# Optimization experiments

Measured on AMD Instinct MI355X. Metric: run time of the kernel, lower is better.

## Reference

```python
import jax, jax.numpy as jnp
import numpy as np
from jax import lax

IMG = 800.0
PRE_NMS = 2000
POST_NMS = 1000
IOU_T = 0.7
BBOX_XFORM_CLIP = float(np.log(1000.0 / 16.0))


def build_anchors():
    # torchvision FPN anchor generator: one size per level, 3 aspect ratios
    strides = [4, 8, 16, 32, 64]
    sizes = [32, 64, 128, 256, 512]
    ratios = [0.5, 1.0, 2.0]
    out = []
    for s, sz in zip(strides, sizes):
        f = int(np.ceil(800 / s))  # feature map side
        base = []
        for r in ratios:
            w = sz * np.sqrt(1.0 / r)
            h = sz * np.sqrt(r)
            base.append([-w / 2, -h / 2, w / 2, h / 2])
        base = np.asarray(base)  # [3,4]
        sx = (np.arange(f) + 0.5) * s
        sy = (np.arange(f) + 0.5) * s
        yy, xx = np.meshgrid(sy, sx, indexing='ij')
        shifts = np.stack([xx, yy, xx, yy], -1).reshape(-1, 1, 4)
        out.append((shifts + base).reshape(-1, 4))
    return np.concatenate(out, 0).astype(np.float32)  # [159882,4]


def setup_inputs() -> dict:
    key = jax.random.key(0)
    k1, k2 = jax.random.split(key)
    B = 16
    anchors = jnp.asarray(build_anchors())
    A = anchors.shape[0]
    scores = jax.random.normal(k1, (B, A), dtype=jnp.float32)
    deltas = jax.random.normal(k2, (B, A, 4), dtype=jnp.float32) * 0.1
    return {"scores": scores, "deltas": deltas, "anchors": anchors}


def decode_boxes(deltas, anchors):
    wa = anchors[:, 2] - anchors[:, 0]
    ha = anchors[:, 3] - anchors[:, 1]
    cxa = anchors[:, 0] + 0.5 * wa
    cya = anchors[:, 1] + 0.5 * ha
    dx, dy = deltas[:, 0], deltas[:, 1]
    dw = jnp.minimum(deltas[:, 2], BBOX_XFORM_CLIP)
    dh = jnp.minimum(deltas[:, 3], BBOX_XFORM_CLIP)
    cx = dx * wa + cxa
    cy = dy * ha + cya
    w = jnp.exp(dw) * wa
    h = jnp.exp(dh) * ha
    boxes = jnp.stack([cx - 0.5 * w, cy - 0.5 * h, cx + 0.5 * w, cy + 0.5 * h], -1)
    return jnp.clip(boxes, 0.0, IMG)


def box_iou(a, b):
    # a: [N,4], b: [M,4]
    area_a = (a[:, 2] - a[:, 0]) * (a[:, 3] - a[:, 1])
    area_b = (b[:, 2] - b[:, 0]) * (b[:, 3] - b[:, 1])
    lt = jnp.maximum(a[:, None, :2], b[None, :, :2])
    rb = jnp.minimum(a[:, None, 2:], b[None, :, 2:])
    wh = jnp.clip(rb - lt, 0.0)
    inter = wh[..., 0] * wh[..., 1]
    return inter / (area_a[:, None] + area_b[None, :] - inter + 1e-9)


def greedy_nms_keep(boxes, iou_t):
    # boxes are sorted by descending score
    K = boxes.shape[0]
    iou = box_iou(boxes, boxes)  # [K,K]
    idx = jnp.arange(K)

    def body(i, keep):
        sup = (iou[i] > iou_t) & keep[i] & (idx > i)
        return keep & ~sup

    return lax.fori_loop(0, K, body, jnp.ones((K,), bool))


def _process_image(scores_i, deltas_i, anchors):
    # top-k pre-NMS on objectness logits (torchvision RPN order)
    top_logits, idx = lax.top_k(scores_i, PRE_NMS)
    boxes = decode_boxes(deltas_i[idx], anchors[idx])  # [PRE,4]
    keep = greedy_nms_keep(boxes, IOU_T)
    masked = jnp.where(keep, top_logits, -jnp.inf)
    kept_logits, idx2 = lax.top_k(masked, POST_NMS)
    kept_boxes = boxes[idx2]
    valid = jnp.isfinite(kept_logits)
    probs = jax.nn.sigmoid(jnp.where(valid, kept_logits, 0.0))
    out_boxes = jnp.where(valid[:, None], kept_boxes, 0.0)
    out_scores = jnp.where(valid, probs, 0.0)
    return jnp.concatenate([out_boxes, out_scores[:, None]], -1)  # [POST,5]


def reference(scores, deltas, anchors):
    return jax.vmap(_process_image, in_axes=(0, 0, None))(scores, deltas, anchors)
```

## Files before the change

### kernel.cpp

```cpp
#include <hip/hip_runtime.h>
#include <math.h>

#define PRE_NMS 2000
#define POST_NMS 1000
#define IOU_T 0.7f
#define IMGSZ 800.0f
#define CAP 6144
#define SORTN 2048
#define NBINS 1024
#define NWORDS 32
#define NSLICE 16
#define MROWS 2048

typedef unsigned long long u64;

__device__ __forceinline__ unsigned key_of(float f) {
    unsigned u = __float_as_uint(f);
    return (u & 0x80000000u) ? ~u : (u | 0x80000000u);
}
__device__ __forceinline__ float inv_key(unsigned k) {
    unsigned u = (k & 0x80000000u) ? (k ^ 0x80000000u) : ~k;
    return __uint_as_float(u);
}

__global__ __launch_bounds__(256) void hist_kernel(
    const float* __restrict__ scores, int A, unsigned* __restrict__ ghist) {
  int b = blockIdx.x, slice = blockIdx.y;
  __shared__ unsigned h[NBINS];
  int tid = threadIdx.x;
  for (int i = tid; i < NBINS; i += 256) h[i] = 0;
  __syncthreads();
  int per = (A + NSLICE - 1) / NSLICE;
  int lo = slice * per, hi = min(lo + per, A);
  const float* sc = scores + (size_t)b * A;
  for (int i = lo + tid; i < hi; i += 256)
    atomicAdd(&h[key_of(sc[i]) >> 22], 1u);
  __syncthreads();
  for (int i = tid; i < NBINS; i += 256)
    if (h[i]) atomicAdd(&ghist[b * NBINS + i], h[i]);
}

__global__ __launch_bounds__(256) void compact_kernel(
    const float* __restrict__ scores, int A, const unsigned* __restrict__ ghist,
    u64* __restrict__ cand, int* __restrict__ cand_cnt, int* __restrict__ T1) {
  int b = blockIdx.x, slice = blockIdx.y;
  int tid = threadIdx.x;
  int lane = tid & 63, wave = tid >> 6;
  __shared__ unsigned sa[2][NBINS];
  __shared__ int sT;
  for (int i = tid; i < NBINS; i += 256) sa[0][i] = ghist[b * NBINS + i];
  __syncthreads();
  int src = 0;
  for (int d = 1; d < NBINS; d <<= 1) {
    for (int i = tid; i < NBINS; i += 256)
      sa[src ^ 1][i] = sa[src][i] + ((i + d < NBINS) ? sa[src][i + d] : 0u);
    __syncthreads();
    src ^= 1;
  }
  for (int i = tid; i < NBINS; i += 256) {
    unsigned v = sa[src][i];
    unsigned nx = (i < NBINS - 1) ? sa[src][i + 1] : 0u;
    if (v >= PRE_NMS && nx < PRE_NMS) sT = i;
  }
  __syncthreads();
  int T = sT;
  if (slice == 0 && tid == 0) T1[b] = T;
  int per = (A + NSLICE - 1) / NSLICE;
  int lo = slice * per, hi = min(lo + per, A);
  const float* sc = scores + (size_t)b * A;
  int cnt = 0;
  for (int i = lo + tid; i < hi; i += 256)
    cnt += ((int)(key_of(sc[i]) >> 22) >= T);
  int pfx = cnt;
  #pragma unroll
  for (int d = 1; d < 64; d <<= 1) {
    int t2 = __shfl_up(pfx, d, 64);
    if (lane >= d) pfx += t2;
  }
  __shared__ int s_wt[4];
  __shared__ int s_base;
  if (lane == 63) s_wt[wave] = pfx;
  __syncthreads();
  if (tid == 0) {
    int tot = s_wt[0] + s_wt[1] + s_wt[2] + s_wt[3];
    int acc = 0;
    #pragma unroll
    for (int w2 = 0; w2 < 4; ++w2) { int t3 = s_wt[w2]; s_wt[w2] = acc; acc += t3; }
    s_base = atomicAdd(&cand_cnt[b], tot);
  }
  __syncthreads();
  int my_off = s_base + s_wt[wave] + (pfx - cnt);
  u64* cb = cand + (size_t)b * CAP;
  for (int i = lo + tid; i < hi; i += 256) {
    unsigned k = key_of(sc[i]);
    if ((int)(k >> 22) >= T) {
      if (my_off < CAP) cb[my_off] = ((u64)k << 32) | (unsigned)(~i);
      my_off++;
    }
  }
}

__global__ __launch_bounds__(1024) void refine_select_kernel(
    const u64* __restrict__ cand, const int* __restrict__ cand_cnt,
    const int* __restrict__ T1,
    u64* __restrict__ gsel, int* __restrict__ sel_cnt) {
  int b = blockIdx.x, tid = threadIdx.x;
  int lane = tid & 63;
  __shared__ unsigned h2[NBINS];
  __shared__ unsigned tmp[NBINS];
  __shared__ int s_above, s_sel, s_T2;
  int n = min(cand_cnt[b], CAP);
  const u64* cb = cand + (size_t)b * CAP;
  h2[tid] = 0;
  if (tid == 0) { s_above = 0; s_sel = 0; }
  __syncthreads();
  int T1v = T1[b];
  int loc = 0;
  for (int i = tid; i < n; i += 1024) {
    unsigned k = (unsigned)(cb[i] >> 32);
    if ((int)(k >> 22) > T1v) loc++;
    else atomicAdd(&h2[(k >> 12) & 1023], 1u);
  }
  for (int d = 32; d; d >>= 1) loc += __shfl_down(loc, d, 64);
  if (lane == 0 && loc) atomicAdd(&s_above, loc);
  __syncthreads();
  unsigned v = h2[tid];
  for (int d = 1; d < NBINS; d <<= 1) {
    tmp[tid] = v;
    __syncthreads();
    if (tid + d < NBINS) v += tmp[tid + d];
    __syncthreads();
  }
  tmp[tid] = v;
  __syncthreads();
  int above = s_above;
  unsigned nextv = (tid < NBINS - 1) ? tmp[tid + 1] : 0u;
  if (above + (int)v >= PRE_NMS && above + (int)nextv < PRE_NMS) s_T2 = tid;
  __syncthreads();
  unsigned thresh20 = ((unsigned)T1v << 10) | (unsigned)s_T2;
  u64* gs = gsel + (size_t)b * SORTN;
  for (int i = tid; i < n; i += 1024) {
    u64 cv = cb[i];
    if ((unsigned)(cv >> 44) >= thresh20) {
      int pos = atomicAdd(&s_sel, 1);
      if (pos < SORTN) gs[pos] = cv;
    }
  }
  __syncthreads();
  if (tid == 0) sel_cnt[b] = min(s_sel, SORTN);
}

__global__ __launch_bounds__(256) void rank_decode_kernel(
    const u64* __restrict__ gsel, const int* __restrict__ sel_cnt,
    const float* __restrict__ deltas, const float* __restrict__ anchors, int A,
    float* __restrict__ boxes, float* __restrict__ topk_logit) {
  int b = blockIdx.x, ci = blockIdx.y;
  int tid = threadIdx.x;
  __shared__ u64 keys[SORTN];
  const u64* gs = gsel + (size_t)b * SORTN;
  int n = sel_cnt[b];
  for (int i = tid; i < SORTN; i += 256)
    keys[i] = (i < n) ? gs[i] : 0ULL;
  __syncthreads();
  int i = ci * 256 + tid;
  u64 my = keys[i];
  int rank = 0;
  const ulonglong2* k2 = (const ulonglong2*)keys;
  #pragma unroll 4
  for (int j = 0; j < SORTN / 2; ++j) {
    ulonglong2 kk = k2[j];
    rank += (kk.x > my) + (kk.y > my);
  }
  if (i < n && rank < PRE_NMS) {
    int a = (int)(~(unsigned)my);
    topk_logit[b * PRE_NMS + rank] = inv_key((unsigned)(my >> 32));
    const float CLIP = 4.135166556742356f;
    float4 dl = ((const float4*)deltas)[(size_t)b * A + a];
    float4 an = ((const float4*)anchors)[a];
    float wa = __fsub_rn(an.z, an.x);
    float ha = __fsub_rn(an.w, an.y);
    float cxa = __fadd_rn(an.x, __fmul_rn(0.5f, wa));
    float cya = __fadd_rn(an.y, __fmul_rn(0.5f, ha));
    float dw = fminf(dl.z, CLIP), dh = fminf(dl.w, CLIP);
    float cx = __fadd_rn(__fmul_rn(dl.x, wa), cxa);
    float cy = __fadd_rn(__fmul_rn(dl.y, ha), cya);
    float w2 = __fmul_rn((float)exp((double)dw), wa);
    float h2f = __fmul_rn((float)exp((double)dh), ha);
    float x1 = __fsub_rn(cx, __fmul_rn(0.5f, w2));
    float y1 = __fsub_rn(cy, __fmul_rn(0.5f, h2f));
    float x2 = __fadd_rn(cx, __fmul_rn(0.5f, w2));
    float y2 = __fadd_rn(cy, __fmul_rn(0.5f, h2f));
    x1 = fminf(fmaxf(x1, 0.f), IMGSZ);
    y1 = fminf(fmaxf(y1, 0.f), IMGSZ);
    x2 = fminf(fmaxf(x2, 0.f), IMGSZ);
    y2 = fminf(fmaxf(y2, 0.f), IMGSZ);
    ((float4*)boxes)[(size_t)b * PRE_NMS + rank] = make_float4(x1, y1, x2, y2);
  }
}

__global__ __launch_bounds__(64) void iou_tile(
    const float* __restrict__ boxes, u64* __restrict__ maskT) {
  int k = blockIdx.x;
  int b = blockIdx.y;
  int wj = (int)((sqrtf(8.0f * k + 1.0f) - 1.0f) * 0.5f);
  while ((wj + 1) * (wj + 2) / 2 <= k) ++wj;
  while (wj * (wj + 1) / 2 > k) --wj;
  int ti = k - wj * (wj + 1) / 2;
  int lane = threadIdx.x;
  int i = ti * 64 + lane;
  const float4* bb = (const float4*)boxes + (size_t)b * PRE_NMS;
  __shared__ float4 sbox[64];
  int jg = wj * 64 + lane;
  sbox[lane] = bb[min(jg, PRE_NMS - 1)];
  float4 A4 = bb[min(i, PRE_NMS - 1)];
  __syncthreads();
  float area_a = __fmul_rn(__fsub_rn(A4.z, A4.x), __fsub_rn(A4.w, A4.y));
  u64 m = 0;
  #pragma unroll 8
  for (int jj = 0; jj < 64; ++jj) {
    float4 Bb = sbox[jj];
    float area_b = __fmul_rn(__fsub_rn(Bb.z, Bb.x), __fsub_rn(Bb.w, Bb.y));
    float ltx = fmaxf(A4.x, Bb.x), lty = fmaxf(A4.y, Bb.y);
    float rbx = fminf(A4.z, Bb.z), rby = fminf(A4.w, Bb.w);
    float iw = fmaxf(__fsub_rn(rbx, ltx), 0.f);
    float ih = fmaxf(__fsub_rn(rby, lty), 0.f);
    float inter = __fmul_rn(iw, ih);
    float denom = __fadd_rn(__fsub_rn(__fadd_rn(area_a, area_b), inter), 1e-9f);
    float iou = inter / denom;
    int j = wj * 64 + jj;
    if (j > i && iou > IOU_T) m |= 1ULL << jj;
  }
  maskT[((size_t)b * NWORDS + wj) * MROWS + i] = m;
}

#define WSTRIDE 65
__global__ __launch_bounds__(256, 1) void nms_scan(
    const u64* __restrict__ maskT, const float* __restrict__ boxes,
    const float* __restrict__ logits, float* __restrict__ out) {
  int b = blockIdx.x;
  int tid = threadIdx.x;
  int wave = tid >> 6, lane = tid & 63;
  __shared__ u64 buf[3][NWORDS * WSTRIDE];
  __shared__ u64 s_keep[NWORDS];
  __shared__ u64 s_cur[2];
  if (tid < NWORDS) s_keep[tid] = (tid == NWORDS - 1) ? 0xFFFFULL : ~0ULL;
  const u64* mb = maskT + (size_t)b * NWORDS * MROWS;
  int w = tid >> 3;
  int sub = tid & 7;
  uint4 nx0, nx1, nx2, nx3;
  {
    const uint4* src = (const uint4*)(mb + (size_t)w * MROWS + sub * 8);
    uint4 a0 = src[0], a1 = src[1], a2 = src[2], a3 = src[3];
    u64* dst = &buf[0][w * WSTRIDE + sub * 8];
    dst[0] = ((u64)a0.y << 32) | a0.x;  dst[1] = ((u64)a0.w << 32) | a0.z;
    dst[2] = ((u64)a1.y << 32) | a1.x;  dst[3] = ((u64)a1.w << 32) | a1.z;
    dst[4] = ((u64)a2.y << 32) | a2.x;  dst[5] = ((u64)a2.w << 32) | a2.z;
    dst[6] = ((u64)a3.y << 32) | a3.x;  dst[7] = ((u64)a3.w << 32) | a3.z;
  }
  if (w >= 1) {
    const uint4* src = (const uint4*)(mb + (size_t)w * MROWS + 64 + sub * 8);
    nx0 = src[0]; nx1 = src[1]; nx2 = src[2]; nx3 = src[3];
  }
  __syncthreads();
  for (int c = 0; c < NWORDS; ++c) {
    if (c + 1 < NWORDS && w >= c + 1) {
      u64* dst = &buf[(c + 1) % 3][w * WSTRIDE + sub * 8];
      dst[0] = ((u64)nx0.y << 32) | nx0.x;  dst[1] = ((u64)nx0.w << 32) | nx0.z;
      dst[2] = ((u64)nx1.y << 32) | nx1.x;  dst[3] = ((u64)nx1.w << 32) | nx1.z;
      dst[4] = ((u64)nx2.y << 32) | nx2.x;  dst[5] = ((u64)nx2.w << 32) | nx2.z;
      dst[6] = ((u64)nx3.y << 32) | nx3.x;  dst[7] = ((u64)nx3.w << 32) | nx3.z;
    }
    if (c + 2 < NWORDS && w >= c + 2) {
      const uint4* src = (const uint4*)(mb + (size_t)w * MROWS + (c + 2) * 64 + sub * 8);
      nx0 = src[0]; nx1 = src[1]; nx2 = src[2]; nx3 = src[3];
    }
    if (wave == 0) {
      u64 diag = buf[c % 3][c * WSTRIDE + lane];
      unsigned dlo = (unsigned)diag, dhi = (unsigned)(diag >> 32);
      u64 k0 = s_keep[c];
      unsigned clo = __builtin_amdgcn_readfirstlane((unsigned)k0);
      unsigned chi = __builtin_amdgcn_readfirstlane((unsigned)(k0 >> 32));
      #pragma unroll
      for (int bb = 0; bb < 32; ++bb) {
        unsigned rlo = __builtin_amdgcn_readlane(dlo, bb);
        unsigned rhi = __builtin_amdgcn_readlane(dhi, bb);
        unsigned msk = 0u - ((clo >> bb) & 1u);
        clo &= ~(rlo & msk);
        chi &= ~(rhi & msk);
      }
      #pragma unroll
      for (int bb = 0; bb < 32; ++bb) {
        unsigned rlo = __builtin_amdgcn_readlane(dlo, bb + 32);
        unsigned rhi = __builtin_amdgcn_readlane(dhi, bb + 32);
        unsigned msk = 0u - ((chi >> bb) & 1u);
        clo &= ~(rlo & msk);
        chi &= ~(rhi & msk);
      }
      u64 cur = ((u64)chi << 32) | clo;
      if (lane == 0) { s_keep[c] = cur; s_cur[c & 1] = cur; }
      if (c + 1 < NWORDS) {
        u64 row = buf[c % 3][(c + 1) * WSTRIDE + lane];
        u64 bit = (cur >> lane) & 1ULL;
        u64 v = row & (0ULL - bit);
        v |= __shfl_xor(v, 1, 64);
        v |= __shfl_xor(v, 2, 64);
        v |= __shfl_xor(v, 4, 64);
        v |= __shfl_xor(v, 8, 64);
        v |= __shfl_xor(v, 16, 64);
        v |= __shfl_xor(v, 32, 64);
        if (lane == 0 && v) atomicAnd(&s_keep[c + 1], ~v);
      }
    } else if (c >= 1) {
      u64 kept = s_cur[(c - 1) & 1];
      int g = lane >> 3, s = lane & 7;
      const u64* bbuf = &buf[(c - 1) % 3][0];
      for (int idx = (wave - 1) + 3 * g; idx < NWORDS - 1 - c; idx += 24) {
        int w2 = c + 1 + idx;
        u64 v = 0;
        #pragma unroll
        for (int k = 0; k < 8; ++k) {
          int r = s + 8 * k;
          u64 bit = (kept >> r) & 1ULL;
          v |= bbuf[w2 * WSTRIDE + r] & (0ULL - bit);
        }
        v |= __shfl_xor(v, 1, 64);
        v |= __shfl_xor(v, 2, 64);
        v |= __shfl_xor(v, 4, 64);
        if (s == 0 && v) atomicAnd(&s_keep[w2], ~v);
      }
    }
    __syncthreads();
  }
  __shared__ int pre[NWORDS];
  __shared__ int s_tot;
  if (tid == 0) {
    int acc = 0;
    for (int ww = 0; ww < NWORDS; ++ww) {
      pre[ww] = acc;
      acc += __popcll(s_keep[ww]);
    }
    s_tot = acc;
  }
  __syncthreads();
  const float* lg_b = logits + b * PRE_NMS;
  const float4* bx_b = (const float4*)boxes + (size_t)b * PRE_NMS;
  for (int i = tid; i < PRE_NMS; i += 256) {
    u64 wv = s_keep[i >> 6];
    if ((wv >> (i & 63)) & 1) {
      int rank = pre[i >> 6] + __popcll(wv & ((1ULL << (i & 63)) - 1ULL));
      if (rank < POST_NMS) {
        float4 bx = bx_b[i];
        float lg = lg_b[i];
        float e = (float)exp(-(double)lg);
        float pp = 1.0f / (1.0f + e);
        float* o = out + ((size_t)b * POST_NMS + rank) * 5;
        o[0] = bx.x; o[1] = bx.y; o[2] = bx.z; o[3] = bx.w; o[4] = pp;
      }
    }
  }
  int tot = s_tot;
  for (int j = tid; j < POST_NMS; j += 256) {
    if (j >= tot) {
      float* o = out + ((size_t)b * POST_NMS + j) * 5;
      o[0] = 0.f; o[1] = 0.f; o[2] = 0.f; o[3] = 0.f; o[4] = 0.f;
    }
  }
}

extern "C" void kernel_launch(void* const* d_in, const int* in_sizes, int n_in,
                              void* d_out, int out_size, void* d_ws, size_t ws_size,
                              hipStream_t stream) {
  const float* scores  = (const float*)d_in[0];
  const float* deltas  = (const float*)d_in[1];
  const float* anchors = (const float*)d_in[2];
  int A = in_sizes[2] / 4;
  int B = in_sizes[0] / A;

  char* ws = (char*)d_ws;
  size_t off = 0;
  auto alloc = [&](size_t bytes) {
    void* p = ws + off;
    off += (bytes + 255) & ~(size_t)255;
    return p;
  };
  unsigned* ghist    = (unsigned*)alloc((size_t)B * NBINS * 4);
  int*      cand_cnt = (int*)alloc((size_t)B * 4);
  size_t zero_bytes = off;
  int*      T1       = (int*)alloc((size_t)B * 4);
  u64*      cand     = (u64*)alloc((size_t)B * CAP * 8);
  u64*      gsel     = (u64*)alloc((size_t)B * SORTN * 8);
  int*      sel_cnt  = (int*)alloc((size_t)B * 4);
  float*    topk_lg  = (float*)alloc((size_t)B * PRE_NMS * 4);
  float*    boxes    = (float*)alloc((size_t)B * PRE_NMS * 16);
  u64*      maskT    = (u64*)alloc((size_t)B * NWORDS * MROWS * 8);

  hipMemsetAsync(ws, 0, zero_bytes, stream);

  hist_kernel<<<dim3(B, NSLICE), 256, 0, stream>>>(scores, A, ghist);
  compact_kernel<<<dim3(B, NSLICE), 256, 0, stream>>>(scores, A, ghist, cand, cand_cnt, T1);
  refine_select_kernel<<<B, 1024, 0, stream>>>(cand, cand_cnt, T1, gsel, sel_cnt);
  rank_decode_kernel<<<dim3(B, SORTN / 256), 256, 0, stream>>>(
      gsel, sel_cnt, deltas, anchors, A, boxes, topk_lg);
  int ntiles = NWORDS * (NWORDS + 1) / 2;
  iou_tile<<<dim3(ntiles, B), 64, 0, stream>>>(boxes, maskT);
  nms_scan<<<B, 256, 0, stream>>>(maskT, boxes, topk_lg, (float*)d_out);
}
```

Baseline: 239.4 us.

## Remove refine kernel and memset via per-slice histograms and candidate slots

Each hist and compact block now writes its own histogram slice to global memory instead of atomically accumulating into a shared one, so the memset is no longer needed. The compact kernel also builds the second-level histogram for the threshold bin and counts candidates above it per slice, writing into fixed per-slice slots. The separate refine/select kernel is folded into rank_decode, which sums the slice histograms, finds the fine threshold and compacts the selected keys into shared memory. This saves one kernel launch and one memset. In exchange, every one of the 8 rank_decode blocks per image redundantly redoes the histogram reduction, scan and candidate compaction, and more than 512 candidates in one slice would be silently truncated.

```diff
diff --git a/kernel.cpp b/kernel.cpp
--- a/kernel.cpp
+++ b/kernel.cpp
@@ -5,11 +5,12 @@
 #define POST_NMS 1000
 #define IOU_T 0.7f
 #define IMGSZ 800.0f
-#define CAP 6144
-#define SORTN 2048
 #define NBINS 1024
 #define NWORDS 32
 #define NSLICE 16
+#define SLOT 512
+#define CSTRIDE (NSLICE * SLOT)
+#define SORTN 2048
 #define MROWS 2048
 
 typedef unsigned long long u64;
@@ -24,7 +25,7 @@
 }
 
 __global__ __launch_bounds__(256) void hist_kernel(
-    const float* __restrict__ scores, int A, unsigned* __restrict__ ghist) {
+    const float* __restrict__ scores, int A, unsigned* __restrict__ ghist_s) {
   int b = blockIdx.x, slice = blockIdx.y;
   __shared__ unsigned h[NBINS];
   int tid = threadIdx.x;
@@ -36,19 +37,28 @@
   for (int i = lo + tid; i < hi; i += 256)
     atomicAdd(&h[key_of(sc[i]) >> 22], 1u);
   __syncthreads();
-  for (int i = tid; i < NBINS; i += 256)
-    if (h[i]) atomicAdd(&ghist[b * NBINS + i], h[i]);
+  unsigned* out = ghist_s + ((size_t)(b * NSLICE + slice) << 10);
+  for (int i = tid; i < NBINS; i += 256) out[i] = h[i];
 }
 
 __global__ __launch_bounds__(256) void compact_kernel(
-    const float* __restrict__ scores, int A, const unsigned* __restrict__ ghist,
-    u64* __restrict__ cand, int* __restrict__ cand_cnt, int* __restrict__ T1) {
+    const float* __restrict__ scores, int A, const unsigned* __restrict__ ghist_s,
+    u64* __restrict__ cand, int* __restrict__ scnt,
+    unsigned* __restrict__ gh2_s, int* __restrict__ above_s, int* __restrict__ T1w) {
   int b = blockIdx.x, slice = blockIdx.y;
   int tid = threadIdx.x;
   int lane = tid & 63, wave = tid >> 6;
   __shared__ unsigned sa[2][NBINS];
+  __shared__ unsigned h2[NBINS];
   __shared__ int sT;
-  for (int i = tid; i < NBINS; i += 256) sa[0][i] = ghist[b * NBINS + i];
+  for (int i = tid; i < NBINS; i += 256) {
+    unsigned s = 0;
+    #pragma unroll 4
+    for (int s16 = 0; s16 < NSLICE; ++s16)
+      s += ghist_s[((size_t)(b * NSLICE + s16) << 10) + i];
+    sa[0][i] = s;
+    h2[i] = 0;
+  }
   __syncthreads();
   int src = 0;
   for (int d = 1; d < NBINS; d <<= 1) {
@@ -64,106 +74,158 @@
   }
   __syncthreads();
   int T = sT;
-  if (slice == 0 && tid == 0) T1[b] = T;
+  if (slice == 0 && tid == 0) T1w[b] = T;
   int per = (A + NSLICE - 1) / NSLICE;
   int lo = slice * per, hi = min(lo + per, A);
   const float* sc = scores + (size_t)b * A;
-  int cnt = 0;
-  for (int i = lo + tid; i < hi; i += 256)
-    cnt += ((int)(key_of(sc[i]) >> 22) >= T);
+  int cnt = 0, abv = 0;
+  for (int i = lo + tid; i < hi; i += 256) {
+    int bin = (int)(key_of(sc[i]) >> 22);
+    cnt += (bin >= T);
+    abv += (bin > T);
+  }
   int pfx = cnt;
   #pragma unroll
   for (int d = 1; d < 64; d <<= 1) {
     int t2 = __shfl_up(pfx, d, 64);
     if (lane >= d) pfx += t2;
   }
+  #pragma unroll
+  for (int d = 32; d; d >>= 1) abv += __shfl_down(abv, d, 64);
   __shared__ int s_wt[4];
-  __shared__ int s_base;
+  __shared__ int s_ab[4];
+  __shared__ int s_tot;
   if (lane == 63) s_wt[wave] = pfx;
+  if (lane == 0) s_ab[wave] = abv;
   __syncthreads();
   if (tid == 0) {
-    int tot = s_wt[0] + s_wt[1] + s_wt[2] + s_wt[3];
     int acc = 0;
     #pragma unroll
     for (int w2 = 0; w2 < 4; ++w2) { int t3 = s_wt[w2]; s_wt[w2] = acc; acc += t3; }
-    s_base = atomicAdd(&cand_cnt[b], tot);
-  }
-  __syncthreads();
-  int my_off = s_base + s_wt[wave] + (pfx - cnt);
-  u64* cb = cand + (size_t)b * CAP;
+    s_tot = acc;
+    above_s[b * NSLICE + slice] = s_ab[0] + s_ab[1] + s_ab[2] + s_ab[3];
+    scnt[b * NSLICE + slice] = min(acc, SLOT);
+  }
+  __syncthreads();
+  int my_off = s_wt[wave] + (pfx - cnt);
+  u64* cb = cand + (size_t)b * CSTRIDE + slice * SLOT;
   for (int i = lo + tid; i < hi; i += 256) {
     unsigned k = key_of(sc[i]);
-    if ((int)(k >> 22) >= T) {
-      if (my_off < CAP) cb[my_off] = ((u64)k << 32) | (unsigned)(~i);
+    int bin = (int)(k >> 22);
+    if (bin >= T) {
+      if (my_off < SLOT) cb[my_off] = ((u64)k << 32) | (unsigned)(~i);
       my_off++;
-    }
-  }
-}
-
-__global__ __launch_bounds__(1024) void refine_select_kernel(
-    const u64* __restrict__ cand, const int* __restrict__ cand_cnt,
-    const int* __restrict__ T1,
-    u64* __restrict__ gsel, int* __restrict__ sel_cnt) {
-  int b = blockIdx.x, tid = threadIdx.x;
-  int lane = tid & 63;
-  __shared__ unsigned h2[NBINS];
-  __shared__ unsigned tmp[NBINS];
-  __shared__ int s_above, s_sel, s_T2;
-  int n = min(cand_cnt[b], CAP);
-  const u64* cb = cand + (size_t)b * CAP;
-  h2[tid] = 0;
-  if (tid == 0) { s_above = 0; s_sel = 0; }
-  __syncthreads();
-  int T1v = T1[b];
-  int loc = 0;
-  for (int i = tid; i < n; i += 1024) {
-    unsigned k = (unsigned)(cb[i] >> 32);
-    if ((int)(k >> 22) > T1v) loc++;
-    else atomicAdd(&h2[(k >> 12) & 1023], 1u);
-  }
-  for (int d = 32; d; d >>= 1) loc += __shfl_down(loc, d, 64);
-  if (lane == 0 && loc) atomicAdd(&s_above, loc);
-  __syncthreads();
-  unsigned v = h2[tid];
-  for (int d = 1; d < NBINS; d <<= 1) {
-    tmp[tid] = v;
-    __syncthreads();
-    if (tid + d < NBINS) v += tmp[tid + d];
-    __syncthreads();
-  }
-  tmp[tid] = v;
-  __syncthreads();
-  int above = s_above;
-  unsigned nextv = (tid < NBINS - 1) ? tmp[tid + 1] : 0u;
-  if (above + (int)v >= PRE_NMS && above + (int)nextv < PRE_NMS) s_T2 = tid;
-  __syncthreads();
-  unsigned thresh20 = ((unsigned)T1v << 10) | (unsigned)s_T2;
-  u64* gs = gsel + (size_t)b * SORTN;
-  for (int i = tid; i < n; i += 1024) {
-    u64 cv = cb[i];
-    if ((unsigned)(cv >> 44) >= thresh20) {
-      int pos = atomicAdd(&s_sel, 1);
-      if (pos < SORTN) gs[pos] = cv;
-    }
-  }
-  __syncthreads();
-  if (tid == 0) sel_cnt[b] = min(s_sel, SORTN);
+      if (bin == T) atomicAdd(&h2[(k >> 12) & 1023], 1u);
+    }
+  }
+  __syncthreads();
+  unsigned* gh = gh2_s + ((size_t)(b * NSLICE + slice) << 10);
+  for (int i = tid; i < NBINS; i += 256) gh[i] = h2[i];
 }
 
 __global__ __launch_bounds__(256) void rank_decode_kernel(
-    const u64* __restrict__ gsel, const int* __restrict__ sel_cnt,
+    const u64* __restrict__ cand, const int* __restrict__ scnt,
+    const unsigned* __restrict__ gh2_s, const int* __restrict__ above_s,
+    const int* __restrict__ T1w,
     const float* __restrict__ deltas, const float* __restrict__ anchors, int A,
     float* __restrict__ boxes, float* __restrict__ topk_logit) {
   int b = blockIdx.x, ci = blockIdx.y;
   int tid = threadIdx.x;
+  int lane = tid & 63, wave = tid >> 6;
+  __shared__ unsigned sa[2][NBINS];
   __shared__ u64 keys[SORTN];
-  const u64* gs = gsel + (size_t)b * SORTN;
-  int n = sel_cnt[b];
+  __shared__ int s_T2, s_tot;
+  __shared__ int s_wt[4];
+  __shared__ int p[NSLICE + 1];
+  __shared__ int sc_l[NSLICE];
+  for (int i = tid; i < NBINS; i += 256) {
+    unsigned s = 0;
+    #pragma unroll 4
+    for (int s16 = 0; s16 < NSLICE; ++s16)
+      s += gh2_s[((size_t)(b * NSLICE + s16) << 10) + i];
+    sa[0][i] = s;
+  }
+  if (tid == 0) {
+    int acc = 0;
+    #pragma unroll
+    for (int s16 = 0; s16 < NSLICE; ++s16) {
+      int c = scnt[b * NSLICE + s16];
+      sc_l[s16] = c;
+      p[s16] = acc;
+      acc += c;
+    }
+    p[NSLICE] = acc;
+  }
+  __syncthreads();
+  int src = 0;
+  for (int d = 1; d < NBINS; d <<= 1) {
+    for (int i = tid; i < NBINS; i += 256)
+      sa[src ^ 1][i] = sa[src][i] + ((i + d < NBINS) ? sa[src][i + d] : 0u);
+    __syncthreads();
+    src ^= 1;
+  }
+  int above = 0;
+  #pragma unroll
+  for (int s16 = 0; s16 < NSLICE; ++s16) above += above_s[b * NSLICE + s16];
+  for (int i = tid; i < NBINS; i += 256) {
+    unsigned v = sa[src][i];
+    unsigned nx = (i < NBINS - 1) ? sa[src][i + 1] : 0u;
+    if (above + (int)v >= PRE_NMS && above + (int)nx < PRE_NMS) s_T2 = i;
+  }
+  __syncthreads();
+  unsigned th20 = ((unsigned)T1w[b] << 10) | (unsigned)s_T2;
+  const u64* cb = cand + (size_t)b * CSTRIDE;
+  int n = p[NSLICE];
+  int chunk = (n + 255) / 256;
+  int st = min(tid * chunk, n), en = min(st + chunk, n);
+  int cnt = 0;
+  {
+    int sl = 0;
+    while (sl < NSLICE && p[sl + 1] <= st) sl++;
+    int idx = st - p[sl];
+    for (int g = st; g < en; ++g) {
+      while (idx >= sc_l[sl]) { sl++; idx = 0; }
+      u64 cv = cb[sl * SLOT + idx];
+      cnt += ((unsigned)(cv >> 44) >= th20);
+      idx++;
+    }
+  }
+  int pfx = cnt;
+  #pragma unroll
+  for (int d = 1; d < 64; d <<= 1) {
+    int t2 = __shfl_up(pfx, d, 64);
+    if (lane >= d) pfx += t2;
+  }
+  if (lane == 63) s_wt[wave] = pfx;
+  __syncthreads();
+  if (tid == 0) {
+    int acc = 0;
+    #pragma unroll
+    for (int w2 = 0; w2 < 4; ++w2) { int t3 = s_wt[w2]; s_wt[w2] = acc; acc += t3; }
+    s_tot = acc;
+  }
+  __syncthreads();
+  int pos = s_wt[wave] + (pfx - cnt);
+  {
+    int sl = 0;
+    while (sl < NSLICE && p[sl + 1] <= st) sl++;
+    int idx = st - p[sl];
+    for (int g = st; g < en; ++g) {
+      while (idx >= sc_l[sl]) { sl++; idx = 0; }
+      u64 cv = cb[sl * SLOT + idx];
+      if ((unsigned)(cv >> 44) >= th20) {
+        if (pos < SORTN) keys[pos] = cv;
+        pos++;
+      }
+      idx++;
+    }
+  }
+  int nsel = min(s_tot, SORTN);
   for (int i = tid; i < SORTN; i += 256)
-    keys[i] = (i < n) ? gs[i] : 0ULL;
-  __syncthreads();
-  int i = ci * 256 + tid;
-  u64 my = keys[i];
+    if (i >= nsel) keys[i] = 0ULL;
+  __syncthreads();
+  int i0 = ci * 256 + tid;
+  u64 my = keys[i0];
   int rank = 0;
   const ulonglong2* k2 = (const ulonglong2*)keys;
   #pragma unroll 4
@@ -171,7 +233,7 @@
     ulonglong2 kk = k2[j];
     rank += (kk.x > my) + (kk.y > my);
   }
-  if (i < n && rank < PRE_NMS) {
+  if (i0 < nsel && rank < PRE_NMS) {
     int a = (int)(~(unsigned)my);
     topk_logit[b * PRE_NMS + rank] = inv_key((unsigned)(my >> 32));
     const float CLIP = 4.135166556742356f;
@@ -332,14 +394,14 @@
     __syncthreads();
   }
   __shared__ int pre[NWORDS];
-  __shared__ int s_tot;
+  __shared__ int s_tot2;
   if (tid == 0) {
     int acc = 0;
     for (int ww = 0; ww < NWORDS; ++ww) {
       pre[ww] = acc;
       acc += __popcll(s_keep[ww]);
     }
-    s_tot = acc;
+    s_tot2 = acc;
   }
   __syncthreads();
   const float* lg_b = logits + b * PRE_NMS;
@@ -358,7 +420,7 @@
       }
     }
   }
-  int tot = s_tot;
+  int tot = s_tot2;
   for (int j = tid; j < POST_NMS; j += 256) {
     if (j >= tot) {
       float* o = out + ((size_t)b * POST_NMS + j) * 5;
@@ -383,24 +445,21 @@
     off += (bytes + 255) & ~(size_t)255;
     return p;
   };
-  unsigned* ghist    = (unsigned*)alloc((size_t)B * NBINS * 4);
-  int*      cand_cnt = (int*)alloc((size_t)B * 4);
-  size_t zero_bytes = off;
-  int*      T1       = (int*)alloc((size_t)B * 4);
-  u64*      cand     = (u64*)alloc((size_t)B * CAP * 8);
-  u64*      gsel     = (u64*)alloc((size_t)B * SORTN * 8);
-  int*      sel_cnt  = (int*)alloc((size_t)B * 4);
-  float*    topk_lg  = (float*)alloc((size_t)B * PRE_NMS * 4);
-  float*    boxes    = (float*)alloc((size_t)B * PRE_NMS * 16);
-  u64*      maskT    = (u64*)alloc((size_t)B * NWORDS * MROWS * 8);
-
-  hipMemsetAsync(ws, 0, zero_bytes, stream);
-
-  hist_kernel<<<dim3(B, NSLICE), 256, 0, stream>>>(scores, A, ghist);
-  compact_kernel<<<dim3(B, NSLICE), 256, 0, stream>>>(scores, A, ghist, cand, cand_cnt, T1);
-  refine_select_kernel<<<B, 1024, 0, stream>>>(cand, cand_cnt, T1, gsel, sel_cnt);
+  unsigned* ghist_s = (unsigned*)alloc((size_t)B * NSLICE * NBINS * 4);
+  unsigned* gh2_s   = (unsigned*)alloc((size_t)B * NSLICE * NBINS * 4);
+  int*      scnt    = (int*)alloc((size_t)B * NSLICE * 4);
+  int*      above_s = (int*)alloc((size_t)B * NSLICE * 4);
+  int*      T1w     = (int*)alloc((size_t)B * 4);
+  u64*      cand    = (u64*)alloc((size_t)B * CSTRIDE * 8);
+  float*    topk_lg = (float*)alloc((size_t)B * PRE_NMS * 4);
+  float*    boxes   = (float*)alloc((size_t)B * PRE_NMS * 16);
+  u64*      maskT   = (u64*)alloc((size_t)B * NWORDS * MROWS * 8);
+
+  hist_kernel<<<dim3(B, NSLICE), 256, 0, stream>>>(scores, A, ghist_s);
+  compact_kernel<<<dim3(B, NSLICE), 256, 0, stream>>>(
+      scores, A, ghist_s, cand, scnt, gh2_s, above_s, T1w);
   rank_decode_kernel<<<dim3(B, SORTN / 256), 256, 0, stream>>>(
-      gsel, sel_cnt, deltas, anchors, A, boxes, topk_lg);
+      cand, scnt, gh2_s, above_s, T1w, deltas, anchors, A, boxes, topk_lg);
   int ntiles = NWORDS * (NWORDS + 1) / 2;
   iou_tile<<<dim3(ntiles, B), 64, 0, stream>>>(boxes, maskT);
   nms_scan<<<B, 256, 0, stream>>>(maskT, boxes, topk_lg, (float*)d_out);
```

New measurement: 247.5 us. 1.03x slower.
